# Performance work log

Measured on AMD Instinct MI355X. Metric: run time of the kernel, lower is better.

Reference implementation:

```python
import jax, jax.numpy as jnp
import numpy as np
import math

B, S, D, H, F, L, V = 2, 2048, 1024, 16, 4096, 3, 32000
DK = D // H
EPS = 1e-6
NEG = -1e9


def layernorm(x, a, b):
    # torch: std(-1) is Bessel-corrected (ddof=1); eps added to std, not var
    mean = x.mean(-1, keepdims=True)
    std = jnp.sqrt(((x - mean) ** 2).sum(-1, keepdims=True) / (x.shape[-1] - 1))
    return a * (x - mean) / (std + EPS) + b


def setup_inputs() -> dict:
    key = jax.random.key(0)
    ks = jax.random.split(key, 12)
    rn = lambda k, shape, s=0.02: jax.random.normal(k, shape, dtype=jnp.float32) * s
    tokens = jax.random.randint(ks[0], (B, S), 0, V, dtype=jnp.int32)
    mask = jnp.ones((B, 1, S), dtype=jnp.int32)
    emb = rn(ks[1], (V, D), 1.0)
    # sinusoidal positional encoding (buffer, matches PositionalEncoding)
    pos = np.arange(S, dtype=np.float32)[:, None]
    div = np.exp(np.arange(0, D, 2, dtype=np.float32) * -(math.log(10000.0) / D))
    pe_np = np.zeros((S, D), np.float32)
    pe_np[:, 0::2] = np.sin(pos * div)
    pe_np[:, 1::2] = np.cos(pos * div)
    pe = jnp.asarray(pe_np)
    return dict(
        tokens=tokens, mask=mask, emb=emb, pe=pe,
        Wq=rn(ks[2], (L, D, D)), bq=jnp.zeros((L, D), jnp.float32),
        Wk=rn(ks[3], (L, D, D)), bk=jnp.zeros((L, D), jnp.float32),
        Wv=rn(ks[4], (L, D, D)), bv=jnp.zeros((L, D), jnp.float32),
        Wo=rn(ks[5], (L, D, D)), bo=jnp.zeros((L, D), jnp.float32),
        w1=rn(ks[6], (L, D, F)), b1=jnp.zeros((L, F), jnp.float32),
        w2=rn(ks[7], (L, F, D)), b2=jnp.zeros((L, D), jnp.float32),
        ln_a=jnp.ones((L, 2, D), jnp.float32), ln_b=jnp.zeros((L, 2, D), jnp.float32),
        fa=jnp.ones((D,), jnp.float32), fb=jnp.zeros((D,), jnp.float32),
    )


def encoder(tokens, mask, emb, pe, Wq, bq, Wk, bk, Wv, bv, Wo, bo,
            w1, b1, w2, b2, ln_a, ln_b, fa, fb):
    x = emb[tokens] * jnp.float32(math.sqrt(D)) + pe[None, :, :]  # [B,S,D]
    m = (mask[:, None, :, :] != 0)  # [B,1,1,S] broadcast over heads and queries
    scale = jnp.float32(1.0 / math.sqrt(DK))
    for l in range(L):
        # --- self-attention sublayer (pre-LN residual) ---
        h = layernorm(x, ln_a[l, 0], ln_b[l, 0])
        q = (h @ Wq[l] + bq[l]).reshape(B, S, H, DK)
        k = (h @ Wk[l] + bk[l]).reshape(B, S, H, DK)
        v = (h @ Wv[l] + bv[l]).reshape(B, S, H, DK)
        scores = jnp.einsum('bqhd,bkhd->bhqk', q, k) * scale
        scores = jnp.where(m, scores, jnp.float32(NEG))
        p = jax.nn.softmax(scores, axis=-1)
        o = jnp.einsum('bhqk,bkhd->bqhd', p, v).reshape(B, S, D)
        x = x + (o @ Wo[l] + bo[l])
        # --- feed-forward sublayer (pre-LN residual) ---
        h = layernorm(x, ln_a[l, 1], ln_b[l, 1])
        x = x + (jax.nn.relu(h @ w1[l] + b1[l]) @ w2[l] + b2[l])
    return layernorm(x, fa, fb)


def reference(tokens, mask, emb, pe, Wq, bq, Wk, bk, Wv, bv, Wo, bo,
              w1, b1, w2, b2, ln_a, ln_b, fa, fb):
    return encoder(tokens, mask, emb, pe, Wq, bq, Wk, bk, Wv, bv, Wo, bo,
                   w1, b1, w2, b2, ln_a, ln_b, fa, fb)
```

## Files before the change

kernel.cpp:

```cpp
#include <hip/hip_runtime.h>
#include <math.h>
#include <stdint.h>

constexpr int kB = 2, kS = 2048, kD = 1024, kH = 16, kF = 4096, kL = 3;
constexpr int kDK = 64;
constexpr int kQKV = 3 * kD;

typedef __attribute__((ext_vector_type(8))) short short8;
typedef __attribute__((ext_vector_type(4))) float floatx4;

__device__ inline float bf2f(unsigned short u) {
  union { uint32_t i; float f; } v; v.i = (uint32_t)u << 16; return v.f;
}
__device__ inline unsigned short f2bf(float x) {
  union { float f; uint32_t i; } v; v.f = x;
  uint32_t r = v.i + 0x7fffu + ((v.i >> 16) & 1u);
  return (unsigned short)(r >> 16);
}

__device__ inline void dma16(const void* g, void* l) {
  __builtin_amdgcn_global_load_lds(
      (const __attribute__((address_space(1))) unsigned int*)g,
      (__attribute__((address_space(3))) unsigned int*)l, 16, 0, 0);
}

__global__ __launch_bounds__(256) void embed_kernel(
    const int* __restrict__ tokens, const float* __restrict__ emb,
    const float* __restrict__ pe, float* __restrict__ x)
{
  int i = blockIdx.x;
  int s = i & (kS - 1);
  int tok = tokens[i];
  const float4* ep = (const float4*)(emb + (size_t)tok * kD);
  const float4* pp = (const float4*)(pe + (size_t)s * kD);
  float4* xp = (float4*)(x + (size_t)i * kD);
  int t = threadIdx.x;
  float4 e = ep[t], p = pp[t];
  xp[t] = make_float4(e.x*32.0f + p.x, e.y*32.0f + p.y,
                      e.z*32.0f + p.z, e.w*32.0f + p.w);
}

__global__ __launch_bounds__(256) void ln_kernel(
    const float* __restrict__ x, const float* __restrict__ ga,
    const float* __restrict__ gb, float* __restrict__ out)
{
  int row = blockIdx.x;
  int t = threadIdx.x;
  int lane = t & 63, wid = t >> 6;
  const float4* xp = (const float4*)(x + (size_t)row * kD);
  float4 v = xp[t];
  float s = v.x + v.y + v.z + v.w;
  #pragma unroll
  for (int o = 32; o; o >>= 1) s += __shfl_xor(s, o);
  __shared__ float red[4];
  if (lane == 0) red[wid] = s;
  __syncthreads();
  float mean = (red[0] + red[1] + red[2] + red[3]) * (1.0f / 1024.0f);
  float4 d = make_float4(v.x - mean, v.y - mean, v.z - mean, v.w - mean);
  float ss = d.x*d.x + d.y*d.y + d.z*d.z + d.w*d.w;
  #pragma unroll
  for (int o = 32; o; o >>= 1) ss += __shfl_xor(ss, o);
  __syncthreads();
  if (lane == 0) red[wid] = ss;
  __syncthreads();
  float var = (red[0] + red[1] + red[2] + red[3]) * (1.0f / 1023.0f);
  float inv = 1.0f / (sqrtf(var) + 1e-6f);
  float4 a4 = ((const float4*)ga)[t];
  float4 b4 = ((const float4*)gb)[t];
  float4 o4;
  o4.x = a4.x * d.x * inv + b4.x;
  o4.y = a4.y * d.y * inv + b4.y;
  o4.z = a4.z * d.z * inv + b4.z;
  o4.w = a4.w * d.w * inv + b4.w;
  ((float4*)(out + (size_t)row * kD))[t] = o4;
}

__global__ __launch_bounds__(256) void ln_split_kernel(
    const float* __restrict__ x, const float* __restrict__ ga,
    const float* __restrict__ gb, unsigned short* __restrict__ hi,
    unsigned short* __restrict__ lo)
{
  int row = blockIdx.x;
  int t = threadIdx.x;
  int lane = t & 63, wid = t >> 6;
  const float4* xp = (const float4*)(x + (size_t)row * kD);
  float4 v = xp[t];
  float s = v.x + v.y + v.z + v.w;
  #pragma unroll
  for (int o = 32; o; o >>= 1) s += __shfl_xor(s, o);
  __shared__ float red[4];
  if (lane == 0) red[wid] = s;
  __syncthreads();
  float mean = (red[0] + red[1] + red[2] + red[3]) * (1.0f / 1024.0f);
  float4 d = make_float4(v.x - mean, v.y - mean, v.z - mean, v.w - mean);
  float ss = d.x*d.x + d.y*d.y + d.z*d.z + d.w*d.w;
  #pragma unroll
  for (int o = 32; o; o >>= 1) ss += __shfl_xor(ss, o);
  __syncthreads();
  if (lane == 0) red[wid] = ss;
  __syncthreads();
  float var = (red[0] + red[1] + red[2] + red[3]) * (1.0f / 1023.0f);
  float inv = 1.0f / (sqrtf(var) + 1e-6f);
  float4 a4 = ((const float4*)ga)[t];
  float4 b4 = ((const float4*)gb)[t];
  float o0 = a4.x * d.x * inv + b4.x;
  float o1 = a4.y * d.y * inv + b4.y;
  float o2 = a4.z * d.z * inv + b4.z;
  float o3 = a4.w * d.w * inv + b4.w;
  ushort4 h4, l4;
  h4.x = f2bf(o0); l4.x = f2bf(o0 - bf2f(h4.x));
  h4.y = f2bf(o1); l4.y = f2bf(o1 - bf2f(h4.y));
  h4.z = f2bf(o2); l4.z = f2bf(o2 - bf2f(h4.z));
  h4.w = f2bf(o3); l4.w = f2bf(o3 - bf2f(h4.w));
  *(ushort4*)&hi[(size_t)row * kD + 4*t] = h4;
  *(ushort4*)&lo[(size_t)row * kD + 4*t] = l4;
}

__global__ __launch_bounds__(256) void wconv_kernel(
    const float* __restrict__ W, unsigned short* __restrict__ hi,
    unsigned short* __restrict__ lo, int K, int N)
{
  __shared__ float tile[64][65];
  int n0 = blockIdx.x * 64, k0 = blockIdx.y * 64;
  int c = threadIdx.x & 63, r0 = threadIdx.x >> 6;
  #pragma unroll
  for (int p = 0; p < 16; ++p) {
    int r = r0 + 4 * p;
    tile[r][c] = W[(size_t)(k0 + r) * N + n0 + c];
  }
  __syncthreads();
  #pragma unroll
  for (int p = 0; p < 16; ++p) {
    int nn = r0 + 4 * p;
    float xv = tile[c][nn];
    unsigned short h = f2bf(xv);
    size_t o = (size_t)(n0 + nn) * K + k0 + c;
    hi[o] = h;
    lo[o] = f2bf(xv - bf2f(h));
  }
}

template<int TERMS, int OUTMODE, int BN>
__global__ __launch_bounds__(256, 3) void mfma_gemm(
    const unsigned short* __restrict__ Ahi, const unsigned short* __restrict__ Alo,
    const unsigned short* __restrict__ Whi, const unsigned short* __restrict__ Wlo,
    const float* __restrict__ bias, const float* __restrict__ resid,
    void* __restrict__ out, int M, int N, int K)
{
  constexpr int NJ = (BN == 128) ? 4 : 2;

  __shared__ unsigned short sAhi[128 * 32];
  __shared__ unsigned short sBhi[BN * 32];
  __shared__ unsigned short sBlo[BN * 32];
  __shared__ unsigned short sAlo[TERMS == 3 ? 128 * 32 : 64];

  int t = threadIdx.x;
  int lane = t & 63, wv = t >> 6;
  int wm, wn;
  if (BN == 128) { wm = (wv >> 1) * 64; wn = (wv & 1) * 64; }
  else           { wm = (wv & 1) * 64;  wn = (wv >> 1) * 32; }
  int lr = lane & 15, lq = lane >> 4;
  int m0 = blockIdx.y * 128, n0 = blockIdx.x * BN;

  int u = lane >> 2;
  int kq_g = (lane & 3) ^ ((u ^ (u >> 2)) & 3);
  int swv = (lr ^ (lr >> 2)) & 3;

  floatx4 acc[4][NJ];
  #pragma unroll
  for (int i = 0; i < 4; ++i)
    #pragma unroll
    for (int j = 0; j < NJ; ++j) acc[i][j] = (floatx4){0.f, 0.f, 0.f, 0.f};

  for (int k0 = 0; k0 < K; k0 += 32) {
    __syncthreads();
    #pragma unroll
    for (int p = 0; p < 2; ++p) {
      int W = 2 * wv + p;
      size_t ga = (size_t)(m0 + 16 * W + u) * K + k0 + 8 * kq_g;
      dma16(&Ahi[ga], &sAhi[W * 512]);
      if (TERMS == 3) dma16(&Alo[ga], &sAlo[W * 512]);
    }
    if (BN == 128) {
      #pragma unroll
      for (int p = 0; p < 2; ++p) {
        int W = 2 * wv + p;
        size_t gb = (size_t)(n0 + 16 * W + u) * K + k0 + 8 * kq_g;
        dma16(&Whi[gb], &sBhi[W * 512]);
        dma16(&Wlo[gb], &sBlo[W * 512]);
      }
    } else {
      int W = wv;
      size_t gb = (size_t)(n0 + 16 * W + u) * K + k0 + 8 * kq_g;
      dma16(&Whi[gb], &sBhi[W * 512]);
      dma16(&Wlo[gb], &sBlo[W * 512]);
    }
    __syncthreads();

    short8 ah[4], bh[NJ];
    #pragma unroll
    for (int i = 0; i < 4; ++i)
      ah[i] = *(const short8*)&sAhi[(wm + 16*i + lr) * 32 + 8 * (lq ^ swv)];
    #pragma unroll
    for (int j = 0; j < NJ; ++j)
      bh[j] = *(const short8*)&sBhi[(wn + 16*j + lr) * 32 + 8 * (lq ^ swv)];
    #pragma unroll
    for (int i = 0; i < 4; ++i)
      #pragma unroll
      for (int j = 0; j < NJ; ++j)
        acc[i][j] = __builtin_amdgcn_mfma_f32_16x16x32_bf16(ah[i], bh[j], acc[i][j], 0, 0, 0);

    short8 bl[NJ];
    #pragma unroll
    for (int j = 0; j < NJ; ++j)
      bl[j] = *(const short8*)&sBlo[(wn + 16*j + lr) * 32 + 8 * (lq ^ swv)];
    #pragma unroll
    for (int i = 0; i < 4; ++i)
      #pragma unroll
      for (int j = 0; j < NJ; ++j)
        acc[i][j] = __builtin_amdgcn_mfma_f32_16x16x32_bf16(ah[i], bl[j], acc[i][j], 0, 0, 0);

    if (TERMS == 3) {
      short8 al[4];
      #pragma unroll
      for (int i = 0; i < 4; ++i)
        al[i] = *(const short8*)&sAlo[(wm + 16*i + lr) * 32 + 8 * (lq ^ swv)];
      #pragma unroll
      for (int i = 0; i < 4; ++i)
        #pragma unroll
        for (int j = 0; j < NJ; ++j)
          acc[i][j] = __builtin_amdgcn_mfma_f32_16x16x32_bf16(al[i], bh[j], acc[i][j], 0, 0, 0);
    }
  }

  if (OUTMODE == 3) {
    unsigned short* qk  = (unsigned short*)out;
    unsigned short* vTp = (unsigned short*)resid;
    #pragma unroll
    for (int i = 0; i < 4; ++i) {
      #pragma unroll
      for (int j = 0; j < NJ; ++j) {
        int col = n0 + wn + 16*j + lr;
        float bv = bias[col];
        int row0 = m0 + wm + 16*i + 4*lq;
        if (col < 2048) {
          #pragma unroll
          for (int r = 0; r < 4; ++r)
            qk[(size_t)(row0 + r) * 2048 + col] = f2bf(acc[i][j][r] + bv);
        } else {
          ushort4 w;
          w.x = f2bf(acc[i][j][0] + bv);
          w.y = f2bf(acc[i][j][1] + bv);
          w.z = f2bf(acc[i][j][2] + bv);
          w.w = f2bf(acc[i][j][3] + bv);
          int bb = row0 >> 11, s0 = row0 & 2047;
          int hh = (col - 2048) >> 6, dk = (col - 2048) & 63;
          *(ushort4*)&vTp[((size_t)((bb << 4) + hh) * 64 + dk) * 2048 + s0] = w;
        }
      }
    }
    return;
  }

  #pragma unroll
  for (int i = 0; i < 4; ++i) {
    #pragma unroll
    for (int j = 0; j < NJ; ++j) {
      int col = n0 + wn + 16*j + lr;
      float bv = bias[col];
      #pragma unroll
      for (int r = 0; r < 4; ++r) {
        int row = m0 + wm + 16*i + 4*lq + r;
        float val = acc[i][j][r] + bv;
        if (OUTMODE == 0) {
          if (resid) val += resid[(size_t)row * N + col];
          ((float*)out)[(size_t)row * N + col] = val;
        } else if (OUTMODE == 1) {
          ((unsigned short*)out)[(size_t)row * N + col] = f2bf(fmaxf(val, 0.f));
        } else {
          ((unsigned short*)out)[(size_t)row * N + col] = f2bf(val);
        }
      }
    }
  }
}

#define ASTR 72

__global__ __launch_bounds__(256, 4) void attn_kernel(
    const unsigned short* __restrict__ QKg, const unsigned short* __restrict__ vT,
    const int* __restrict__ mask, unsigned short* __restrict__ oHi,
    unsigned short* __restrict__ oLo)
{
  __shared__ unsigned short Qs[64 * 64];
  __shared__ unsigned short Ks[64 * 64];
  __shared__ unsigned short Vs[64 * 64];
  __shared__ unsigned short Ps[64 * ASTR];

  int bi = blockIdx.x;
  int bh = bi & 31;
  int qt = bi >> 5;
  int h = bh & 15, b = bh >> 4;
  int q0 = qt * 64;
  int t = threadIdx.x;
  int lane = t & 63, wv = t >> 6;
  int lr = lane & 15, lq = lane >> 4;
  int wq = wv * 16;

  const size_t qbase = (size_t)b * kS * 2048 + (size_t)h * kDK;
  const size_t kbase = qbase + 1024;
  const size_t vbase = (size_t)(b * kH + h) * 64 * 2048;
  const size_t hout  = (size_t)b * kS * kD + (size_t)h * kDK;

  #pragma unroll
  for (int p = 0; p < 2; ++p) {
    int idx = t + 256 * p;
    int row = idx >> 3, cg = (idx & 7) ^ (row & 7);
    dma16(&QKg[qbase + (size_t)(q0 + row) * 2048 + 8 * cg],
          &Qs[(p * 256 + wv * 64) * 8]);
  }

  floatx4 Oacc[4];
  float m_i[4], l_i[4];
  #pragma unroll
  for (int r = 0; r < 4; ++r) { m_i[r] = -3.0e38f; l_i[r] = 0.0f; }
  #pragma unroll
  for (int j = 0; j < 4; ++j) Oacc[j] = (floatx4){0.f, 0.f, 0.f, 0.f};

  for (int k0 = 0; k0 < kS; k0 += 64) {
    __syncthreads();
    #pragma unroll
    for (int p = 0; p < 2; ++p) {
      int idx = t + 256 * p;
      int row = idx >> 3, cg = (idx & 7) ^ (row & 7);
      dma16(&QKg[kbase + (size_t)(k0 + row) * 2048 + 8 * cg],
            &Ks[(p * 256 + wv * 64) * 8]);
      dma16(&vT[vbase + (size_t)row * 2048 + k0 + 8 * cg],
            &Vs[(p * 256 + wv * 64) * 8]);
    }
    int mv[4];
    #pragma unroll
    for (int j = 0; j < 4; ++j) mv[j] = mask[b * kS + k0 + 16*j + lr];
    __syncthreads();

    floatx4 sac[4];
    #pragma unroll
    for (int j = 0; j < 4; ++j) sac[j] = (floatx4){0.f, 0.f, 0.f, 0.f};
    #pragma unroll
    for (int ks = 0; ks < 2; ++ks) {
      int cs = ((4 * ks + lq) ^ (lr & 7)) * 8;
      short8 af = *(const short8*)&Qs[(wq + lr) * 64 + cs];
      short8 bf[4];
      #pragma unroll
      for (int j = 0; j < 4; ++j)
        bf[j] = *(const short8*)&Ks[(16*j + lr) * 64 + cs];
      #pragma unroll
      for (int j = 0; j < 4; ++j)
        sac[j] = __builtin_amdgcn_mfma_f32_16x16x32_bf16(af, bf[j], sac[j], 0, 0, 0);
    }

    #pragma unroll
    for (int j = 0; j < 4; ++j) {
      #pragma unroll
      for (int r = 0; r < 4; ++r) sac[j][r] *= 0.125f;
      if (mv[j] == 0)
        #pragma unroll
        for (int r = 0; r < 4; ++r) sac[j][r] = -1e9f;
    }

    float alf[4];
    #pragma unroll
    for (int r = 0; r < 4; ++r) {
      float mx = fmaxf(fmaxf(sac[0][r], sac[1][r]),
                       fmaxf(sac[2][r], sac[3][r]));
      #pragma unroll
      for (int o = 1; o < 16; o <<= 1) mx = fmaxf(mx, __shfl_xor(mx, o));
      float newm = fmaxf(m_i[r], mx);
      float rs = 0.0f;
      #pragma unroll
      for (int j = 0; j < 4; ++j) {
        float e = __expf(sac[j][r] - newm);
        sac[j][r] = e; rs += e;
      }
      #pragma unroll
      for (int o = 1; o < 16; o <<= 1) rs += __shfl_xor(rs, o);
      alf[r] = __expf(m_i[r] - newm);
      l_i[r] = l_i[r] * alf[r] + rs;
      m_i[r] = newm;
    }

    #pragma unroll
    for (int j = 0; j < 4; ++j)
      #pragma unroll
      for (int r = 0; r < 4; ++r)
        Ps[(wq + 4*lq + r) * ASTR + 16*j + lr] = f2bf(sac[j][r]);

    #pragma unroll
    for (int j = 0; j < 4; ++j)
      #pragma unroll
      for (int r = 0; r < 4; ++r) Oacc[j][r] *= alf[r];

    #pragma unroll
    for (int ks = 0; ks < 2; ++ks) {
      int cs = ((4 * ks + lq) ^ (lr & 7)) * 8;
      short8 pa = *(const short8*)&Ps[(wq + lr) * ASTR + 32*ks + 8*lq];
      short8 vb[4];
      #pragma unroll
      for (int j = 0; j < 4; ++j)
        vb[j] = *(const short8*)&Vs[(16*j + lr) * 64 + cs];
      #pragma unroll
      for (int j = 0; j < 4; ++j)
        Oacc[j] = __builtin_amdgcn_mfma_f32_16x16x32_bf16(pa, vb[j], Oacc[j], 0, 0, 0);
    }
  }

  float inv[4];
  #pragma unroll
  for (int r = 0; r < 4; ++r) inv[r] = 1.0f / l_i[r];
  #pragma unroll
  for (int j = 0; j < 4; ++j)
    #pragma unroll
    for (int r = 0; r < 4; ++r) {
      int row = q0 + wq + 4*lq + r;
      float val = Oacc[j][r] * inv[r];
      unsigned short hv = f2bf(val);
      unsigned short lv = f2bf(val - bf2f(hv));
      size_t addr = hout + (size_t)row * kD + 16*j + lr;
      oHi[addr] = hv;
      oLo[addr] = lv;
    }
}

extern "C" void kernel_launch(void* const* d_in, const int* in_sizes, int n_in,
                              void* d_out, int out_size, void* d_ws, size_t ws_size,
                              hipStream_t stream) {
  const int*   tokens = (const int*)d_in[0];
  const int*   mask   = (const int*)d_in[1];
  const float* emb    = (const float*)d_in[2];
  const float* pe     = (const float*)d_in[3];
  const float* Wq     = (const float*)d_in[4];
  const float* bq     = (const float*)d_in[5];
  const float* Wk     = (const float*)d_in[6];
  const float* bk     = (const float*)d_in[7];
  const float* Wv     = (const float*)d_in[8];
  const float* bv     = (const float*)d_in[9];
  const float* Wo     = (const float*)d_in[10];
  const float* bo     = (const float*)d_in[11];
  const float* w1     = (const float*)d_in[12];
  const float* b1     = (const float*)d_in[13];
  const float* w2     = (const float*)d_in[14];
  const float* b2     = (const float*)d_in[15];
  const float* ln_a   = (const float*)d_in[16];
  const float* ln_b   = (const float*)d_in[17];
  const float* fa     = (const float*)d_in[18];
  const float* fb     = (const float*)d_in[19];
  float* out = (float*)d_out;
  char*  ws  = (char*)d_ws;

  const int T = kB * kS;
  constexpr size_t MB = 1024 * 1024;

  float*          x     = (float*)(ws);
  unsigned short* hHi   = (unsigned short*)(ws + 16 * MB);
  unsigned short* hLo   = (unsigned short*)(ws + 24 * MB);
  unsigned short* qk    = (unsigned short*)(ws + 32 * MB);
  unsigned short* vT    = (unsigned short*)(ws + 48 * MB);
  float*          bqkv  = (float*)(ws + 56 * MB);
  unsigned short* fpln  = (unsigned short*)(ws + 32 * MB);
  char*           Wbuf  = ws + 64 * MB;

  unsigned short* qkv_hi = (unsigned short*)(Wbuf);
  unsigned short* qkv_lo = (unsigned short*)(Wbuf + 6 * MB);
  unsigned short* so_hi  = (unsigned short*)(Wbuf + 12 * MB);
  unsigned short* so_lo  = (unsigned short*)(Wbuf + 14 * MB);
  unsigned short* ffn_hi = (unsigned short*)(Wbuf + 16 * MB);
  unsigned short* ffn_lo = (unsigned short*)(Wbuf + 24 * MB);

  dim3 blk(256);
  embed_kernel<<<T, blk, 0, stream>>>(tokens, emb, pe, x);

  for (int l = 0; l < kL; ++l) {
    const float* Wql = Wq + (size_t)l * kD * kD;
    const float* Wkl = Wk + (size_t)l * kD * kD;
    const float* Wvl = Wv + (size_t)l * kD * kD;
    const float* Wol = Wo + (size_t)l * kD * kD;
    const float* w1l = w1 + (size_t)l * kD * kF;
    const float* w2l = w2 + (size_t)l * kF * kD;

    wconv_kernel<<<dim3(kD/64, kD/64), blk, 0, stream>>>(
        Wql, qkv_hi,                 qkv_lo,                 kD, kD);
    wconv_kernel<<<dim3(kD/64, kD/64), blk, 0, stream>>>(
        Wkl, qkv_hi + (size_t)kD*kD, qkv_lo + (size_t)kD*kD, kD, kD);
    wconv_kernel<<<dim3(kD/64, kD/64), blk, 0, stream>>>(
        Wvl, qkv_hi + (size_t)2*kD*kD, qkv_lo + (size_t)2*kD*kD, kD, kD);
    wconv_kernel<<<dim3(kD/64, kD/64), blk, 0, stream>>>(Wol, so_hi, so_lo, kD, kD);
    hipMemcpyAsync(bqkv,          bq + (size_t)l*kD, kD*4, hipMemcpyDeviceToDevice, stream);
    hipMemcpyAsync(bqkv + kD,     bk + (size_t)l*kD, kD*4, hipMemcpyDeviceToDevice, stream);
    hipMemcpyAsync(bqkv + 2*kD,   bv + (size_t)l*kD, kD*4, hipMemcpyDeviceToDevice, stream);

    ln_split_kernel<<<T, blk, 0, stream>>>(x, ln_a + (size_t)l * 2 * kD,
                                           ln_b + (size_t)l * 2 * kD, hHi, hLo);
    mfma_gemm<3,3,128><<<dim3(kQKV/128, T/128), blk, 0, stream>>>(
        hHi, hLo, qkv_hi, qkv_lo, bqkv, (const float*)vT, qk, T, kQKV, kD);
    attn_kernel<<<kB * kH * (kS / 64), blk, 0, stream>>>(
        qk, vT, mask, hHi, hLo);
    mfma_gemm<3,0,64><<<dim3(kD/64, T/128), blk, 0, stream>>>(
        hHi, hLo, so_hi, so_lo, bo + (size_t)l * kD, x, x, T, kD, kD);

    ln_split_kernel<<<T, blk, 0, stream>>>(x, ln_a + (size_t)l * 2 * kD + kD,
                                           ln_b + (size_t)l * 2 * kD + kD, hHi, hLo);
    wconv_kernel<<<dim3(kF/64, kD/64), blk, 0, stream>>>(w1l, ffn_hi, ffn_lo, kD, kF);
    mfma_gemm<3,1,128><<<dim3(kF/128, T/128), blk, 0, stream>>>(
        hHi, hLo, ffn_hi, ffn_lo, b1 + (size_t)l * kF, nullptr, fpln, T, kF, kD);
    wconv_kernel<<<dim3(kD/64, kF/64), blk, 0, stream>>>(w2l, ffn_hi, ffn_lo, kF, kD);
    mfma_gemm<2,0,64><<<dim3(kD/64, T/128), blk, 0, stream>>>(
        fpln, nullptr, ffn_hi, ffn_lo, b2 + (size_t)l * kD, x, x, T, kD, kF);
  }

  ln_kernel<<<T, blk, 0, stream>>>(x, fa, fb, out);
}
```

Before: 1.732 ms.

## Use lazy max rescaling, exp2 softmax, and MFMA row sums in attention

Reworks the online softmax in the attention kernel. The scale is folded into an exp2 exponent via FMA. The running max is only updated, with shuffles and O rescaling, when some lane's new max exceeds the stored one by more than a threshold in log2 space. The per-row sum is accumulated by an extra MFMA against a ones vector instead of shuffle reductions, and P is packed with v_cvt_pk_bf16_f32. This removes most of the shuffle reductions and rescale work per tile. In exchange, the exponentials can reach up to 2^8 before the bf16 conversion, and the row sum now uses bf16-rounded probabilities.

```diff
diff --git a/kernel.cpp b/kernel.cpp
--- a/kernel.cpp
+++ b/kernel.cpp
@@ -286,6 +286,7 @@
 }
 
 #define ASTR 72
+#define CL2E 0.18033688011112042f
 
 __global__ __launch_bounds__(256, 4) void attn_kernel(
     const unsigned short* __restrict__ QKg, const unsigned short* __restrict__ vT,
@@ -320,10 +321,15 @@
           &Qs[(p * 256 + wv * 64) * 8]);
   }
 
+  short8 ones;
+  #pragma unroll
+  for (int e = 0; e < 8; ++e) ones[e] = (short)0x3F80;
+
   floatx4 Oacc[4];
-  float m_i[4], l_i[4];
-  #pragma unroll
-  for (int r = 0; r < 4; ++r) { m_i[r] = -3.0e38f; l_i[r] = 0.0f; }
+  floatx4 lacc = (floatx4){0.f, 0.f, 0.f, 0.f};
+  float m_raw[4], msc[4];
+  #pragma unroll
+  for (int r = 0; r < 4; ++r) { m_raw[r] = -3.0e38f; msc[r] = -3.0e38f * CL2E; }
   #pragma unroll
   for (int j = 0; j < 4; ++j) Oacc[j] = (floatx4){0.f, 0.f, 0.f, 0.f};
 
@@ -360,50 +366,56 @@
     }
 
     #pragma unroll
-    for (int j = 0; j < 4; ++j) {
-      #pragma unroll
-      for (int r = 0; r < 4; ++r) sac[j][r] *= 0.125f;
+    for (int j = 0; j < 4; ++j)
       if (mv[j] == 0)
         #pragma unroll
-        for (int r = 0; r < 4; ++r) sac[j][r] = -1e9f;
-    }
-
-    float alf[4];
+        for (int r = 0; r < 4; ++r) sac[j][r] = -3.0e38f;
+
+    float pm[4];
+    int ok = 1;
     #pragma unroll
     for (int r = 0; r < 4; ++r) {
-      float mx = fmaxf(fmaxf(sac[0][r], sac[1][r]),
-                       fmaxf(sac[2][r], sac[3][r]));
-      #pragma unroll
-      for (int o = 1; o < 16; o <<= 1) mx = fmaxf(mx, __shfl_xor(mx, o));
-      float newm = fmaxf(m_i[r], mx);
-      float rs = 0.0f;
-      #pragma unroll
-      for (int j = 0; j < 4; ++j) {
-        float e = __expf(sac[j][r] - newm);
-        sac[j][r] = e; rs += e;
+      pm[r] = fmaxf(fmaxf(sac[0][r], sac[1][r]),
+                    fmaxf(sac[2][r], sac[3][r]));
+      ok &= (__builtin_fmaf(pm[r], CL2E, -msc[r]) <= 8.0f) ? 1 : 0;
+    }
+    if (!__all(ok)) {
+      #pragma unroll
+      for (int r = 0; r < 4; ++r) {
+        float mx = pm[r];
+        #pragma unroll
+        for (int o = 1; o < 16; o <<= 1) mx = fmaxf(mx, __shfl_xor(mx, o));
+        float newm = fmaxf(m_raw[r], mx);
+        float nmsc = newm * CL2E;
+        float alf = __builtin_exp2f(msc[r] - nmsc);
+        m_raw[r] = newm; msc[r] = nmsc;
+        lacc[r] *= alf;
+        #pragma unroll
+        for (int j = 0; j < 4; ++j) Oacc[j][r] *= alf;
       }
-      #pragma unroll
-      for (int o = 1; o < 16; o <<= 1) rs += __shfl_xor(rs, o);
-      alf[r] = __expf(m_i[r] - newm);
-      l_i[r] = l_i[r] * alf[r] + rs;
-      m_i[r] = newm;
-    }
-
-    #pragma unroll
-    for (int j = 0; j < 4; ++j)
-      #pragma unroll
-      for (int r = 0; r < 4; ++r)
-        Ps[(wq + 4*lq + r) * ASTR + 16*j + lr] = f2bf(sac[j][r]);
-
-    #pragma unroll
-    for (int j = 0; j < 4; ++j)
-      #pragma unroll
-      for (int r = 0; r < 4; ++r) Oacc[j][r] *= alf[r];
+    }
+
+    #pragma unroll
+    for (int r = 0; r < 4; ++r) {
+      float e0 = __builtin_exp2f(__builtin_fmaf(sac[0][r], CL2E, -msc[r]));
+      float e1 = __builtin_exp2f(__builtin_fmaf(sac[1][r], CL2E, -msc[r]));
+      float e2 = __builtin_exp2f(__builtin_fmaf(sac[2][r], CL2E, -msc[r]));
+      float e3 = __builtin_exp2f(__builtin_fmaf(sac[3][r], CL2E, -msc[r]));
+      uint32_t u01, u23;
+      asm("v_cvt_pk_bf16_f32 %0, %1, %2" : "=v"(u01) : "v"(e0), "v"(e1));
+      asm("v_cvt_pk_bf16_f32 %0, %1, %2" : "=v"(u23) : "v"(e2), "v"(e3));
+      int row = wq + 4*lq + r;
+      Ps[row * ASTR +      lr] = (unsigned short)u01;
+      Ps[row * ASTR + 16 + lr] = (unsigned short)(u01 >> 16);
+      Ps[row * ASTR + 32 + lr] = (unsigned short)u23;
+      Ps[row * ASTR + 48 + lr] = (unsigned short)(u23 >> 16);
+    }
 
     #pragma unroll
     for (int ks = 0; ks < 2; ++ks) {
       int cs = ((4 * ks + lq) ^ (lr & 7)) * 8;
       short8 pa = *(const short8*)&Ps[(wq + lr) * ASTR + 32*ks + 8*lq];
+      lacc = __builtin_amdgcn_mfma_f32_16x16x32_bf16(pa, ones, lacc, 0, 0, 0);
       short8 vb[4];
       #pragma unroll
       for (int j = 0; j < 4; ++j)
@@ -416,7 +428,7 @@
 
   float inv[4];
   #pragma unroll
-  for (int r = 0; r < 4; ++r) inv[r] = 1.0f / l_i[r];
+  for (int r = 0; r < 4; ++r) inv[r] = 1.0f / lacc[r];
   #pragma unroll
   for (int j = 0; j < 4; ++j)
     #pragma unroll
```

Result: faster. 1.633 ms (-5.7%).
